# Optimization experiments

Hardware: AMD Instinct MI355X
Metric: run time of the kernel (lower is better)

The kernel has to match this reference:

```python
import jax, jax.numpy as jnp
import numpy as np

B, S, H, L = 4, 1024, 1024, 4
NH, NKV, HD = 16, 8, 64
F, V, W = 3072, 32000, 12
THETA = 1000000.0
EPS = 1e-6
NEG = -1e9


def _rms(x, w):
    return (x * jax.lax.rsqrt(jnp.mean(jnp.square(x), axis=-1, keepdims=True) + EPS)) * w


def _rotate_half(x):
    x1, x2 = jnp.split(x, 2, axis=-1)
    return jnp.concatenate([-x2, x1], axis=-1)


def setup_inputs() -> dict:
    key = jax.random.key(0)
    ks = jax.random.split(key, 16)
    s = 0.02
    return {
        'input_ids': jax.random.randint(ks[0], (B, S), 0, V),
        'attention_mask': jnp.ones((B, S), dtype=jnp.int32),
        'embed': jax.random.normal(ks[1], (V, H), jnp.float32) * s,
        'wq': jax.random.normal(ks[2], (L, H, NH * HD), jnp.float32) * s,
        'wk': jax.random.normal(ks[3], (L, H, NKV * HD), jnp.float32) * s,
        'wv': jax.random.normal(ks[4], (L, H, NKV * HD), jnp.float32) * s,
        'wo': jax.random.normal(ks[5], (L, NH * HD, H), jnp.float32) * s,
        'q_norm_w': jnp.ones((L, HD), jnp.float32),
        'k_norm_w': jnp.ones((L, HD), jnp.float32),
        'ln1': jnp.ones((L, H), jnp.float32),
        'ln2': jnp.ones((L, H), jnp.float32),
        'w_gate': jax.random.normal(ks[6], (L, H, F), jnp.float32) * s,
        'w_up': jax.random.normal(ks[7], (L, H, F), jnp.float32) * s,
        'w_down': jax.random.normal(ks[8], (L, F, H), jnp.float32) * s,
        'final_norm': jnp.ones((H,), jnp.float32),
    }


def _forward(embed, wq, wk, wv, wo, q_norm_w, k_norm_w, ln1, ln2,
             w_gate, w_up, w_down, final_norm, input_ids, attention_mask):
    h = embed[input_ids]                                   # [B,S,H]
    # rotary embeddings (Qwen3 style, theta=1e6)
    pos = jnp.arange(S, dtype=jnp.float32)
    inv_freq = 1.0 / (THETA ** (jnp.arange(0, HD, 2, dtype=jnp.float32) / HD))
    freqs = pos[:, None] * inv_freq[None, :]               # [S, HD/2]
    emb = jnp.concatenate([freqs, freqs], axis=-1)         # [S, HD]
    cos = jnp.cos(emb)[None, :, None, :]
    sin = jnp.sin(emb)[None, :, None, :]
    # masks: full = expanded (non-causal) padding mask; sliding = +/-W band
    pad = (1.0 - attention_mask.astype(jnp.float32))[:, None, None, :] * NEG
    idx = jnp.arange(S)
    band = jnp.abs(idx[:, None] - idx[None, :]) <= W       # [S,S]
    full_mask = jnp.broadcast_to(pad, (B, 1, S, S))
    slide_mask = jnp.where(band[None, None], full_mask, NEG)
    scale = 1.0 / np.sqrt(HD).astype(np.float32)
    for l in range(L):
        mask = full_mask if l % 2 == 0 else slide_mask     # attention_type dispatch
        x = _rms(h, ln1[l])
        q = _rms((x @ wq[l]).reshape(B, S, NH, HD), q_norm_w[l])
        k = _rms((x @ wk[l]).reshape(B, S, NKV, HD), k_norm_w[l])
        v = (x @ wv[l]).reshape(B, S, NKV, HD)
        q = q * cos + _rotate_half(q) * sin
        k = k * cos + _rotate_half(k) * sin
        rep = NH // NKV                                    # GQA expand
        k = jnp.repeat(k, rep, axis=2)
        v = jnp.repeat(v, rep, axis=2)
        scores = jnp.einsum('bqhd,bkhd->bhqk', q, k) * scale + mask
        p = jax.nn.softmax(scores, axis=-1)
        attn = jnp.einsum('bhqk,bkhd->bqhd', p, v).reshape(B, S, NH * HD)
        h = h + attn @ wo[l]
        x = _rms(h, ln2[l])
        h = h + (jax.nn.silu(x @ w_gate[l]) * (x @ w_up[l])) @ w_down[l]
    return _rms(h, final_norm)


def reference(input_ids, attention_mask, embed, wq, wk, wv, wo, q_norm_w, k_norm_w,
              ln1, ln2, w_gate, w_up, w_down, final_norm):
    return _forward(embed, wq, wk, wv, wo, q_norm_w, k_norm_w, ln1, ln2,
                    w_gate, w_up, w_down, final_norm, input_ids, attention_mask)
```

## Files before the change

### kernel.cpp

```cpp
#include <hip/hip_runtime.h>
#include <math.h>

#define BB 4
#define SS 1024
#define HH 1024
#define LL 4
#define NHH 16
#define NKV 8
#define HD 64
#define FF 3072
#define WW 12
#define NEG_INF (-1e9f)

typedef __attribute__((ext_vector_type(8))) short bf16x8;
typedef __attribute__((ext_vector_type(4))) float f32x4;
typedef __attribute__((ext_vector_type(16))) float f32x16;
typedef __attribute__((ext_vector_type(8))) unsigned short u16x8;

__device__ __forceinline__ unsigned short f2bf(float f) {
    union { float f; unsigned int u; } v; v.f = f;
    unsigned int r = (v.u + 0x7fffu + ((v.u >> 16) & 1u)) >> 16;
    return (unsigned short)r;
}
__device__ __forceinline__ float bf2f(unsigned short u) {
    union { unsigned int u; float f; } v; v.u = ((unsigned int)u) << 16;
    return v.f;
}
__device__ __forceinline__ unsigned int pkbf(float lo, float hi) {
    return (unsigned int)f2bf(lo) | ((unsigned int)f2bf(hi) << 16);
}
__device__ __forceinline__ void gll16(const void* g, void* l) {
    __builtin_amdgcn_global_load_lds((const __attribute__((address_space(1))) void*)g,
                                     (__attribute__((address_space(3))) void*)l, 16, 0, 0);
}

__global__ __launch_bounds__(256) void k_embed(const int* __restrict__ ids,
                                               const float* __restrict__ embed,
                                               float* __restrict__ h) {
    int row = blockIdx.x, tid = threadIdx.x;
    int id = ids[row];
    ((float4*)(h + (size_t)row * HH))[tid] = ((const float4*)(embed + (size_t)id * HH))[tid];
}

__global__ __launch_bounds__(256) void k_rms(const float* __restrict__ in,
                                             const float* __restrict__ w,
                                             float* __restrict__ out) {
    __shared__ float red[4];
    int row = blockIdx.x, tid = threadIdx.x;
    float4 v = ((const float4*)(in + (size_t)row * HH))[tid];
    float ss = v.x * v.x + v.y * v.y + v.z * v.z + v.w * v.w;
#pragma unroll
    for (int off = 1; off < 64; off <<= 1) ss += __shfl_xor(ss, off);
    if ((tid & 63) == 0) red[tid >> 6] = ss;
    __syncthreads();
    float tot = red[0] + red[1] + red[2] + red[3];
    float scale = rsqrtf(tot * (1.0f / HH) + 1e-6f);
    float4 wv = ((const float4*)w)[tid];
    float4 o;
    o.x = v.x * scale * wv.x; o.y = v.y * scale * wv.y;
    o.z = v.z * scale * wv.z; o.w = v.w * scale * wv.w;
    ((float4*)(out + (size_t)row * HH))[tid] = o;
}

__global__ __launch_bounds__(256) void k_rms_bf16(const float* __restrict__ in,
                                                  const float* __restrict__ w,
                                                  unsigned short* __restrict__ out) {
    __shared__ float red[4];
    int row = blockIdx.x, tid = threadIdx.x;
    float4 v = ((const float4*)(in + (size_t)row * HH))[tid];
    float ss = v.x * v.x + v.y * v.y + v.z * v.z + v.w * v.w;
#pragma unroll
    for (int off = 1; off < 64; off <<= 1) ss += __shfl_xor(ss, off);
    if ((tid & 63) == 0) red[tid >> 6] = ss;
    __syncthreads();
    float tot = red[0] + red[1] + red[2] + red[3];
    float scale = rsqrtf(tot * (1.0f / HH) + 1e-6f);
    float4 wv = ((const float4*)w)[tid];
    ushort4 o;
    o.x = f2bf(v.x * scale * wv.x); o.y = f2bf(v.y * scale * wv.y);
    o.z = f2bf(v.z * scale * wv.z); o.w = f2bf(v.w * scale * wv.w);
    *(ushort4*)&out[(size_t)row * HH + tid * 4] = o;
}

__global__ __launch_bounds__(256) void k_cast_t(const float* __restrict__ W,
                                                unsigned short* __restrict__ Wt,
                                                int N, int K) {
    __shared__ float t[64][65];
    int n0 = blockIdx.x * 64, k0 = blockIdx.y * 64;
    int tid = threadIdx.x;
    int r = tid >> 4;
    int c4 = (tid & 15) * 4;
#pragma unroll
    for (int e = 0; e < 4; ++e) {
        int kk = r + e * 16;
        float4 vv = *(const float4*)&W[(size_t)(k0 + kk) * N + n0 + c4];
        t[c4 + 0][kk] = vv.x;
        t[c4 + 1][kk] = vv.y;
        t[c4 + 2][kk] = vv.z;
        t[c4 + 3][kk] = vv.w;
    }
    __syncthreads();
#pragma unroll
    for (int e = 0; e < 4; ++e) {
        int nn = r + e * 16;
        ushort4 o;
        o.x = f2bf(t[nn][c4 + 0]);
        o.y = f2bf(t[nn][c4 + 1]);
        o.z = f2bf(t[nn][c4 + 2]);
        o.w = f2bf(t[nn][c4 + 3]);
        *(ushort4*)&Wt[(size_t)(n0 + nn) * K + k0 + c4] = o;
    }
}

template <int EPI>
__device__ __forceinline__ void mgemm_core(const unsigned short* __restrict__ A,
                                           const unsigned short* __restrict__ Bt,
                                           void* __restrict__ Cv,
                                           int N, int K, int bm, int bn) {
    __shared__ unsigned short As[128 * 32];
    __shared__ unsigned short Bs[128 * 32];
    int tid = threadIdx.x;
    int w = tid >> 6, l = tid & 63;
    int wr = (w >> 1) * 64, wc = (w & 1) * 64;

    f32x4 acc[4][4] = {};

    for (int k0 = 0; k0 < K; k0 += 32) {
        __syncthreads();
#pragma unroll
        for (int i = 0; i < 2; ++i) {
            int cb = i * 256 + w * 64;
            int c = cb + l;
            const unsigned short* ga = A + (size_t)(bm + (c >> 2)) * K + k0 + (c & 3) * 8;
            const unsigned short* gb = Bt + (size_t)(bn + (c >> 2)) * K + k0 + (c & 3) * 8;
            gll16(ga, As + cb * 8);
            gll16(gb, Bs + cb * 8);
        }
        __syncthreads();

        bf16x8 af[4], bfr[4];
#pragma unroll
        for (int i = 0; i < 4; ++i) {
            int m = wr + i * 16 + (l & 15);
            af[i] = *(const bf16x8*)&As[m * 32 + (l >> 4) * 8];
            int n = wc + i * 16 + (l & 15);
            bfr[i] = *(const bf16x8*)&Bs[n * 32 + (l >> 4) * 8];
        }
#pragma unroll
        for (int i = 0; i < 4; ++i)
#pragma unroll
            for (int j = 0; j < 4; ++j)
                acc[i][j] = __builtin_amdgcn_mfma_f32_16x16x32_bf16(af[i], bfr[j], acc[i][j], 0, 0, 0);
    }

#pragma unroll
    for (int i = 0; i < 4; ++i) {
        int rbase = bm + wr + i * 16 + (l >> 4) * 4;
#pragma unroll
        for (int j = 0; j < 4; ++j) {
            int col = bn + wc + j * 16 + (l & 15);
#pragma unroll
            for (int r = 0; r < 4; ++r) {
                size_t off = (size_t)(rbase + r) * N + col;
                if (EPI == 0) ((float*)Cv)[off] = acc[i][j][r];
                else if (EPI == 1) ((float*)Cv)[off] += acc[i][j][r];
                else ((unsigned short*)Cv)[off] = f2bf(acc[i][j][r]);
            }
        }
    }
}

template <int EPI>
__global__ __launch_bounds__(256) void k_mgemm(const unsigned short* __restrict__ A,
                                               const unsigned short* __restrict__ Bt,
                                               void* __restrict__ C,
                                               int N, int K) {
    mgemm_core<EPI>(A, Bt, C, N, K, blockIdx.y * 128, blockIdx.x * 128);
}

__global__ __launch_bounds__(256) void k_mgemm_qkv(const unsigned short* __restrict__ A,
                                                   const unsigned short* __restrict__ wqt,
                                                   const unsigned short* __restrict__ wkt,
                                                   const unsigned short* __restrict__ wvt,
                                                   float* __restrict__ q,
                                                   float* __restrict__ k,
                                                   unsigned short* __restrict__ v) {
    int nt = blockIdx.x;
    if (nt < 8)       mgemm_core<0>(A, wqt, q, 1024, 1024, blockIdx.y * 128, nt * 128);
    else if (nt < 12) mgemm_core<0>(A, wkt, k, 512, 1024, blockIdx.y * 128, (nt - 8) * 128);
    else              mgemm_core<2>(A, wvt, v, 512, 1024, blockIdx.y * 128, (nt - 12) * 128);
}

__global__ __launch_bounds__(256) void k_mgemm_gu(const unsigned short* __restrict__ A,
                                                  const unsigned short* __restrict__ wgt,
                                                  const unsigned short* __restrict__ wut,
                                                  unsigned short* __restrict__ g,
                                                  unsigned short* __restrict__ u) {
    int nt = blockIdx.x;
    const unsigned short* Bt = (nt < 24) ? wgt : wut;
    unsigned short* C = (nt < 24) ? g : u;
    int bn = (nt < 24 ? nt : nt - 24) * 128;
    mgemm_core<2>(A, Bt, C, 3072, 1024, blockIdx.y * 128, bn);
}

__global__ __launch_bounds__(256) void k_qknorm_rope(const float* __restrict__ qk,
                                                     unsigned short* __restrict__ out,
                                                     const float* __restrict__ nw,
                                                     int nheads) {
    int tid = threadIdx.x;
    int w = tid >> 6, lane = tid & 63;
    int gid = blockIdx.x * 4 + w;
    int row = gid / nheads;
    int pos = row & (SS - 1);
    size_t base = (size_t)gid * HD;
    float xv = qk[base + lane];
    float ss = xv * xv;
#pragma unroll
    for (int off = 1; off < 64; off <<= 1) ss += __shfl_xor(ss, off);
    float scale = rsqrtf(ss * (1.0f / HD) + 1e-6f);
    float xn = xv * scale * nw[lane];
    int j = lane & 31;
    float inv_freq = powf(1.0e6f, -(float)j * (1.0f / 32.0f));
    float f = (float)pos * inv_freq;
    float c = cosf(f), s = sinf(f);
    float partner = __shfl_xor(xn, 32);
    float rot = (lane < 32) ? -partner : partner;
    out[base + lane] = f2bf(xn * c + rot * s);
}

__global__ __launch_bounds__(256) void k_mattn(const unsigned short* __restrict__ q,
                                               const unsigned short* __restrict__ k,
                                               const unsigned short* __restrict__ v,
                                               const int* __restrict__ amask,
                                               unsigned short* __restrict__ out,
                                               int sliding) {
    __shared__ __align__(16) char smem[18432];
    unsigned short* Klds = (unsigned short*)smem;
    unsigned int*   VtU  = (unsigned int*)(smem + 8192);
    float* mlds          = (float*)(smem + 17152);
    unsigned short* Olds = (unsigned short*)smem;

    const int b = blockIdx.z, head = blockIdx.y, q0 = blockIdx.x * 128;
    const int kvh = head >> 1;
    const int tid = threadIdx.x, w = tid >> 6, lane = tid & 63;
    const int h = lane >> 5, ln31 = lane & 31;
    const int qg = q0 + w * 32 + ln31;
    const float sscale = 0.125f;

    bf16x8 qf[4];
    const unsigned short* qrow = q + (size_t)(b * SS + qg) * 1024 + head * 64;
#pragma unroll
    for (int c = 0; c < 4; ++c) qf[c] = *(const bf16x8*)(qrow + c * 16 + h * 8);

    f32x16 O0 = {}, O1 = {};
    float m = -3.4e38f, l_sum = 0.0f;

    int t_lo = 0, t_hi = (SS >> 6) - 1;
    if (sliding) {
        int lo = q0 - WW; if (lo < 0) lo = 0;
        int hi = q0 + 127 + WW; if (hi > SS - 1) hi = SS - 1;
        t_lo = lo >> 6; t_hi = hi >> 6;
    }

    const int vd = tid & 63, vw = tid >> 6;

    for (int t = t_lo; t <= t_hi; ++t) {
        int kv0 = t << 6;
        __syncthreads();
        if (tid < 64) mlds[tid] = amask[b * SS + kv0 + tid] ? 0.0f : NEG_INF;
#pragma unroll
        for (int i = 0; i < 2; ++i) {
            int slot = i * 256 + w * 64 + lane;
            int row = slot >> 3, u = slot & 7;
            int ug = u ^ (row & 7);
            const unsigned short* src = k + (size_t)(b * SS + kv0 + row) * 512 + kvh * 64 + ug * 8;
            gll16(src, Klds + (size_t)slot * 8);
        }
        {
            const unsigned short* vsrc = v + (size_t)(b * SS + kv0 + vw * 16) * 512 + kvh * 64 + vd;
            unsigned short tmp[16];
#pragma unroll
            for (int kk = 0; kk < 16; ++kk) tmp[kk] = vsrc[(size_t)kk * 512];
#pragma unroll
            for (int j = 0; j < 8; ++j)
                VtU[vd * 35 + vw * 8 + j] =
                    (unsigned int)tmp[2 * j] | ((unsigned int)tmp[2 * j + 1] << 16);
        }
        __syncthreads();

        f32x16 a0 = {}, a1 = {};
#pragma unroll
        for (int c = 0; c < 4; ++c) {
            int u = (2 * c + h) ^ (ln31 & 7);
            bf16x8 k0 = *(const bf16x8*)&Klds[ln31 * 64 + u * 8];
            bf16x8 k1 = *(const bf16x8*)&Klds[(32 + ln31) * 64 + u * 8];
            a0 = __builtin_amdgcn_mfma_f32_32x32x16_bf16(k0, qf[c], a0, 0, 0, 0);
            a1 = __builtin_amdgcn_mfma_f32_32x32x16_bf16(k1, qf[c], a1, 0, 0, 0);
        }

        float tmax = -3.4e38f;
#pragma unroll
        for (int r = 0; r < 16; ++r) {
            int kl = (r & 3) + 8 * (r >> 2) + 4 * h;
            float mv0 = mlds[kl], mv1 = mlds[32 + kl];
            if (sliding) {
                int d0 = qg - (kv0 + kl); if (d0 < 0) d0 = -d0;
                int d1 = qg - (kv0 + 32 + kl); if (d1 < 0) d1 = -d1;
                if (d0 > WW) mv0 = NEG_INF;
                if (d1 > WW) mv1 = NEG_INF;
            }
            a0[r] = a0[r] * sscale + mv0;
            a1[r] = a1[r] * sscale + mv1;
            tmax = fmaxf(tmax, fmaxf(a0[r], a1[r]));
        }
        tmax = fmaxf(tmax, __shfl_xor(tmax, 32));
        float nm = fmaxf(m, tmax);
        float corr = __expf(m - nm);
        float tsum = 0.0f;
#pragma unroll
        for (int r = 0; r < 16; ++r) {
            a0[r] = __expf(a0[r] - nm);
            a1[r] = __expf(a1[r] - nm);
            tsum += a0[r] + a1[r];
        }
        tsum += __shfl_xor(tsum, 32);
        l_sum = l_sum * corr + tsum;
#pragma unroll
        for (int r = 0; r < 16; ++r) { O0[r] *= corr; O1[r] *= corr; }
        m = nm;

#pragma unroll
        for (int s = 0; s < 2; ++s) {
#pragma unroll
            for (int c2 = 0; c2 < 2; ++c2) {
                float p0v = s ? a1[8 * c2 + 0] : a0[8 * c2 + 0];
                float p1v = s ? a1[8 * c2 + 1] : a0[8 * c2 + 1];
                float p2v = s ? a1[8 * c2 + 2] : a0[8 * c2 + 2];
                float p3v = s ? a1[8 * c2 + 3] : a0[8 * c2 + 3];
                float p4v = s ? a1[8 * c2 + 4] : a0[8 * c2 + 4];
                float p5v = s ? a1[8 * c2 + 5] : a0[8 * c2 + 5];
                float p6v = s ? a1[8 * c2 + 6] : a0[8 * c2 + 6];
                float p7v = s ? a1[8 * c2 + 7] : a0[8 * c2 + 7];
                unsigned int A0 = pkbf(p0v, p1v);
                unsigned int A1 = pkbf(p2v, p3v);
                unsigned int A2 = pkbf(p4v, p5v);
                unsigned int A3 = pkbf(p6v, p7v);
                unsigned int pA0 = (unsigned int)__shfl_xor((int)A0, 32);
                unsigned int pA1 = (unsigned int)__shfl_xor((int)A1, 32);
                unsigned int pA2 = (unsigned int)__shfl_xor((int)A2, 32);
                unsigned int pA3 = (unsigned int)__shfl_xor((int)A3, 32);
                union { unsigned int u[4]; bf16x8 v; } pf;
                pf.u[0] = h ? pA2 : A0;
                pf.u[1] = h ? pA3 : A1;
                pf.u[2] = h ? A2 : pA0;
                pf.u[3] = h ? A3 : pA1;
#pragma unroll
                for (int dt = 0; dt < 2; ++dt) {
                    int base = (dt * 32 + ln31) * 35 + s * 16 + c2 * 8 + h * 4;
                    union { unsigned int u[4]; bf16x8 v; } vf;
                    vf.u[0] = VtU[base + 0];
                    vf.u[1] = VtU[base + 1];
                    vf.u[2] = VtU[base + 2];
                    vf.u[3] = VtU[base + 3];
                    if (dt == 0) O0 = __builtin_amdgcn_mfma_f32_32x32x16_bf16(vf.v, pf.v, O0, 0, 0, 0);
                    else         O1 = __builtin_amdgcn_mfma_f32_32x32x16_bf16(vf.v, pf.v, O1, 0, 0, 0);
                }
            }
        }
    }

    __syncthreads();
    float rl = 1.0f / l_sum;
    unsigned short* myO = Olds + w * 2240;
#pragma unroll
    for (int dt = 0; dt < 2; ++dt)
#pragma unroll
        for (int r = 0; r < 16; ++r) {
            int d = dt * 32 + (r & 3) + 8 * (r >> 2) + 4 * h;
            float val = (dt ? O1[r] : O0[r]) * rl;
            myO[ln31 * 70 + d] = f2bf(val);
        }
    int qr = lane >> 1, half = lane & 1;
    const unsigned int* osrc = (const unsigned int*)Olds + (size_t)w * 1120 + qr * 35 + half * 16;
    unsigned int vals[16];
#pragma unroll
    for (int j = 0; j < 16; ++j) vals[j] = osrc[j];
    unsigned short* dst = out + (size_t)(b * SS + q0 + w * 32 + qr) * 1024 + head * 64 + half * 32;
#pragma unroll
    for (int j = 0; j < 4; ++j)
        ((uint4*)dst)[j] = make_uint4(vals[4 * j], vals[4 * j + 1], vals[4 * j + 2], vals[4 * j + 3]);
}

__global__ __launch_bounds__(256) void k_silu_bf16(unsigned short* __restrict__ g,
                                                   const unsigned short* __restrict__ u) {
    int i = blockIdx.x * 256 + threadIdx.x;
    u16x8 gv = ((const u16x8*)g)[i];
    u16x8 uv = ((const u16x8*)u)[i];
    u16x8 o;
#pragma unroll
    for (int j = 0; j < 8; ++j) {
        float gf = bf2f(gv[j]), uf = bf2f(uv[j]);
        o[j] = f2bf(gf / (1.0f + __expf(-gf)) * uf);
    }
    ((u16x8*)g)[i] = o;
}

extern "C" void kernel_launch(void* const* d_in, const int* in_sizes, int n_in,
                              void* d_out, int out_size, void* d_ws, size_t ws_size,
                              hipStream_t stream) {
    const int* input_ids = (const int*)d_in[0];
    const int* amask     = (const int*)d_in[1];
    const float* embed   = (const float*)d_in[2];
    const float* wq      = (const float*)d_in[3];
    const float* wk      = (const float*)d_in[4];
    const float* wv      = (const float*)d_in[5];
    const float* wo      = (const float*)d_in[6];
    const float* qnw     = (const float*)d_in[7];
    const float* knw     = (const float*)d_in[8];
    const float* ln1     = (const float*)d_in[9];
    const float* ln2     = (const float*)d_in[10];
    const float* wg      = (const float*)d_in[11];
    const float* wu      = (const float*)d_in[12];
    const float* wd      = (const float*)d_in[13];
    const float* fnorm   = (const float*)d_in[14];
    float* out = (float*)d_out;

    const int ROWS = BB * SS;
    float* h  = (float*)d_ws;
    float* qb = h + (size_t)ROWS * HH;
    float* kb = qb + (size_t)ROWS * HH;
    unsigned short* xb  = (unsigned short*)(kb + (size_t)ROWS * (NKV * HD));
    unsigned short* qbf = xb + (size_t)ROWS * HH;
    unsigned short* kbf = qbf + (size_t)ROWS * HH;
    unsigned short* vbf = kbf + (size_t)ROWS * (NKV * HD);
    unsigned short* gbf = vbf + (size_t)ROWS * (NKV * HD);
    unsigned short* ubf = gbf + (size_t)ROWS * FF;
    unsigned short* wbf = ubf + (size_t)ROWS * FF;

    const size_t OQ = 0, OK_ = 1048576, OV = 1572864, OO = 2097152,
                 OG = 3145728, OU = 6291456, OD = 9437184;

    k_embed<<<ROWS, 256, 0, stream>>>(input_ids, embed, h);

    for (int l = 0; l < LL; ++l) {
        const float* wq_l = wq + (size_t)l * HH * (NHH * HD);
        const float* wk_l = wk + (size_t)l * HH * (NKV * HD);
        const float* wv_l = wv + (size_t)l * HH * (NKV * HD);
        const float* wo_l = wo + (size_t)l * (NHH * HD) * HH;
        const float* wg_l = wg + (size_t)l * HH * FF;
        const float* wu_l = wu + (size_t)l * HH * FF;
        const float* wd_l = wd + (size_t)l * FF * HH;

        k_cast_t<<<dim3(16, 16), 256, 0, stream>>>(wq_l, wbf + OQ, 1024, 1024);
        k_cast_t<<<dim3(8, 16),  256, 0, stream>>>(wk_l, wbf + OK_, 512, 1024);
        k_cast_t<<<dim3(8, 16),  256, 0, stream>>>(wv_l, wbf + OV, 512, 1024);
        k_cast_t<<<dim3(16, 16), 256, 0, stream>>>(wo_l, wbf + OO, 1024, 1024);
        k_cast_t<<<dim3(48, 16), 256, 0, stream>>>(wg_l, wbf + OG, 3072, 1024);
        k_cast_t<<<dim3(48, 16), 256, 0, stream>>>(wu_l, wbf + OU, 3072, 1024);
        k_cast_t<<<dim3(16, 48), 256, 0, stream>>>(wd_l, wbf + OD, 1024, 3072);

        k_rms_bf16<<<ROWS, 256, 0, stream>>>(h, ln1 + l * HH, xb);

        k_mgemm_qkv<<<dim3(16, 32), 256, 0, stream>>>(xb, wbf + OQ, wbf + OK_, wbf + OV,
                                                      qb, kb, vbf);

        k_qknorm_rope<<<ROWS * NHH / 4, 256, 0, stream>>>(qb, qbf, qnw + l * HD, NHH);
        k_qknorm_rope<<<ROWS * NKV / 4, 256, 0, stream>>>(kb, kbf, knw + l * HD, NKV);

        k_mattn<<<dim3(SS / 128, NHH, BB), 256, 0, stream>>>(qbf, kbf, vbf, amask, xb, l & 1);

        k_mgemm<1><<<dim3(8, 32), 256, 0, stream>>>(xb, wbf + OO, h, 1024, 1024);

        k_rms_bf16<<<ROWS, 256, 0, stream>>>(h, ln2 + l * HH, xb);

        k_mgemm_gu<<<dim3(48, 32), 256, 0, stream>>>(xb, wbf + OG, wbf + OU, gbf, ubf);

        k_silu_bf16<<<ROWS * FF / 8 / 256, 256, 0, stream>>>(gbf, ubf);

        k_mgemm<1><<<dim3(8, 32), 256, 0, stream>>>(gbf, wbf + OD, h, 1024, 3072);
    }

    k_rms<<<ROWS, 256, 0, stream>>>(h, fnorm, out);
}
```

Baseline: 1.571 ms.

## Split-K the wo and down GEMMs, fuse residual add into RMSNorm, merge weight casts

The output-projection and down-projection GEMMs are split along K into 2 and 3 parts. Each part writes float partials into scratch buffers that are no longer live (qb, gbf, ubf, part of wbf), which raises the block count above the 256-tile grid. A new fused kernel adds the partials to the residual stream and applies the next RMSNorm, including the first norm of the next layer and the final norm. The seven per-layer weight cast/transpose launches are merged into one launch. The cost is extra partial-buffer traffic and tighter buffer aliasing, which is fragile if the layout ever changes.

```diff
diff --git a/kernel.cpp b/kernel.cpp
--- a/kernel.cpp
+++ b/kernel.cpp
@@ -12,6 +12,14 @@
 #define WW 12
 #define NEG_INF (-1e9f)
 
+#define OQ  0
+#define OK_ 1048576
+#define OV  1572864
+#define OO  2097152
+#define OG  3145728
+#define OU  6291456
+#define OD  9437184
+
 typedef __attribute__((ext_vector_type(8))) short bf16x8;
 typedef __attribute__((ext_vector_type(4))) float f32x4;
 typedef __attribute__((ext_vector_type(16))) float f32x16;
@@ -40,26 +48,6 @@
     int row = blockIdx.x, tid = threadIdx.x;
     int id = ids[row];
     ((float4*)(h + (size_t)row * HH))[tid] = ((const float4*)(embed + (size_t)id * HH))[tid];
-}
-
-__global__ __launch_bounds__(256) void k_rms(const float* __restrict__ in,
-                                             const float* __restrict__ w,
-                                             float* __restrict__ out) {
-    __shared__ float red[4];
-    int row = blockIdx.x, tid = threadIdx.x;
-    float4 v = ((const float4*)(in + (size_t)row * HH))[tid];
-    float ss = v.x * v.x + v.y * v.y + v.z * v.z + v.w * v.w;
-#pragma unroll
-    for (int off = 1; off < 64; off <<= 1) ss += __shfl_xor(ss, off);
-    if ((tid & 63) == 0) red[tid >> 6] = ss;
-    __syncthreads();
-    float tot = red[0] + red[1] + red[2] + red[3];
-    float scale = rsqrtf(tot * (1.0f / HH) + 1e-6f);
-    float4 wv = ((const float4*)w)[tid];
-    float4 o;
-    o.x = v.x * scale * wv.x; o.y = v.y * scale * wv.y;
-    o.z = v.z * scale * wv.z; o.w = v.w * scale * wv.w;
-    ((float4*)(out + (size_t)row * HH))[tid] = o;
 }
 
 __global__ __launch_bounds__(256) void k_rms_bf16(const float* __restrict__ in,
@@ -82,11 +70,68 @@
     *(ushort4*)&out[(size_t)row * HH + tid * 4] = o;
 }
 
-__global__ __launch_bounds__(256) void k_cast_t(const float* __restrict__ W,
-                                                unsigned short* __restrict__ Wt,
-                                                int N, int K) {
+template <int NP, int BF16OUT>
+__global__ __launch_bounds__(256) void k_rms_add(float* __restrict__ h,
+                                                 const float* __restrict__ p0,
+                                                 const float* __restrict__ p1,
+                                                 const float* __restrict__ p2,
+                                                 const float* __restrict__ w,
+                                                 void* __restrict__ outx) {
+    __shared__ float red[4];
+    int row = blockIdx.x, tid = threadIdx.x;
+    size_t base = (size_t)row * HH;
+    float4 v = ((const float4*)(h + base))[tid];
+    float4 a = ((const float4*)(p0 + base))[tid];
+    v.x += a.x; v.y += a.y; v.z += a.z; v.w += a.w;
+    if (NP > 1) {
+        float4 b = ((const float4*)(p1 + base))[tid];
+        v.x += b.x; v.y += b.y; v.z += b.z; v.w += b.w;
+    }
+    if (NP > 2) {
+        float4 c = ((const float4*)(p2 + base))[tid];
+        v.x += c.x; v.y += c.y; v.z += c.z; v.w += c.w;
+    }
+    ((float4*)(h + base))[tid] = v;
+    float ss = v.x * v.x + v.y * v.y + v.z * v.z + v.w * v.w;
+#pragma unroll
+    for (int off = 1; off < 64; off <<= 1) ss += __shfl_xor(ss, off);
+    if ((tid & 63) == 0) red[tid >> 6] = ss;
+    __syncthreads();
+    float tot = red[0] + red[1] + red[2] + red[3];
+    float scale = rsqrtf(tot * (1.0f / HH) + 1e-6f);
+    float4 wv = ((const float4*)w)[tid];
+    float rx = v.x * scale * wv.x, ry = v.y * scale * wv.y;
+    float rz = v.z * scale * wv.z, rw = v.w * scale * wv.w;
+    if (BF16OUT) {
+        ushort4 o;
+        o.x = f2bf(rx); o.y = f2bf(ry); o.z = f2bf(rz); o.w = f2bf(rw);
+        *(ushort4*)&((unsigned short*)outx)[base + tid * 4] = o;
+    } else {
+        float4 o; o.x = rx; o.y = ry; o.z = rz; o.w = rw;
+        ((float4*)((float*)outx + base))[tid] = o;
+    }
+}
+
+__global__ __launch_bounds__(256) void k_cast_all(const float* __restrict__ wq,
+                                                  const float* __restrict__ wk,
+                                                  const float* __restrict__ wv,
+                                                  const float* __restrict__ wo,
+                                                  const float* __restrict__ wg,
+                                                  const float* __restrict__ wu,
+                                                  const float* __restrict__ wd,
+                                                  unsigned short* __restrict__ wbf) {
     __shared__ float t[64][65];
-    int n0 = blockIdx.x * 64, k0 = blockIdx.y * 64;
+    int tI = blockIdx.x;
+    const float* W; unsigned short* Wt; int N, K, local;
+    if (tI < 256)       { W = wq; Wt = wbf + OQ;  N = 1024; K = 1024; local = tI; }
+    else if (tI < 384)  { W = wk; Wt = wbf + OK_; N = 512;  K = 1024; local = tI - 256; }
+    else if (tI < 512)  { W = wv; Wt = wbf + OV;  N = 512;  K = 1024; local = tI - 384; }
+    else if (tI < 768)  { W = wo; Wt = wbf + OO;  N = 1024; K = 1024; local = tI - 512; }
+    else if (tI < 1536) { W = wg; Wt = wbf + OG;  N = 3072; K = 1024; local = tI - 768; }
+    else if (tI < 2304) { W = wu; Wt = wbf + OU;  N = 3072; K = 1024; local = tI - 1536; }
+    else                { W = wd; Wt = wbf + OD;  N = 1024; K = 3072; local = tI - 2304; }
+    int tn = N >> 6;
+    int n0 = (local % tn) * 64, k0 = (local / tn) * 64;
     int tid = threadIdx.x;
     int r = tid >> 4;
     int c4 = (tid & 15) * 4;
@@ -116,7 +161,8 @@
 __device__ __forceinline__ void mgemm_core(const unsigned short* __restrict__ A,
                                            const unsigned short* __restrict__ Bt,
                                            void* __restrict__ Cv,
-                                           int N, int K, int bm, int bn) {
+                                           int N, int K, int lda, int ldb,
+                                           int bm, int bn) {
     __shared__ unsigned short As[128 * 32];
     __shared__ unsigned short Bs[128 * 32];
     int tid = threadIdx.x;
@@ -131,8 +177,8 @@
         for (int i = 0; i < 2; ++i) {
             int cb = i * 256 + w * 64;
             int c = cb + l;
-            const unsigned short* ga = A + (size_t)(bm + (c >> 2)) * K + k0 + (c & 3) * 8;
-            const unsigned short* gb = Bt + (size_t)(bn + (c >> 2)) * K + k0 + (c & 3) * 8;
+            const unsigned short* ga = A + (size_t)(bm + (c >> 2)) * lda + k0 + (c & 3) * 8;
+            const unsigned short* gb = Bt + (size_t)(bn + (c >> 2)) * ldb + k0 + (c & 3) * 8;
             gll16(ga, As + cb * 8);
             gll16(gb, Bs + cb * 8);
         }
@@ -170,12 +216,18 @@
     }
 }
 
-template <int EPI>
-__global__ __launch_bounds__(256) void k_mgemm(const unsigned short* __restrict__ A,
-                                               const unsigned short* __restrict__ Bt,
-                                               void* __restrict__ C,
-                                               int N, int K) {
-    mgemm_core<EPI>(A, Bt, C, N, K, blockIdx.y * 128, blockIdx.x * 128);
+template <int PARTS>
+__global__ __launch_bounds__(256) void k_mgemm_splitk(const unsigned short* __restrict__ A,
+                                                      const unsigned short* __restrict__ Bt,
+                                                      float* __restrict__ p0,
+                                                      float* __restrict__ p1,
+                                                      float* __restrict__ p2,
+                                                      int N, int Ktot) {
+    int part = blockIdx.z;
+    int Kp = Ktot / PARTS;
+    float* C = (part == 0) ? p0 : (part == 1 ? p1 : p2);
+    mgemm_core<0>(A + part * Kp, Bt + part * Kp, C, N, Kp, Ktot, Ktot,
+                  blockIdx.y * 128, blockIdx.x * 128);
 }
 
 __global__ __launch_bounds__(256) void k_mgemm_qkv(const unsigned short* __restrict__ A,
@@ -186,9 +238,9 @@
                                                    float* __restrict__ k,
                                                    unsigned short* __restrict__ v) {
     int nt = blockIdx.x;
-    if (nt < 8)       mgemm_core<0>(A, wqt, q, 1024, 1024, blockIdx.y * 128, nt * 128);
-    else if (nt < 12) mgemm_core<0>(A, wkt, k, 512, 1024, blockIdx.y * 128, (nt - 8) * 128);
-    else              mgemm_core<2>(A, wvt, v, 512, 1024, blockIdx.y * 128, (nt - 12) * 128);
+    if (nt < 8)       mgemm_core<0>(A, wqt, q, 1024, 1024, 1024, 1024, blockIdx.y * 128, nt * 128);
+    else if (nt < 12) mgemm_core<0>(A, wkt, k, 512, 1024, 1024, 1024, blockIdx.y * 128, (nt - 8) * 128);
+    else              mgemm_core<2>(A, wvt, v, 512, 1024, 1024, 1024, blockIdx.y * 128, (nt - 12) * 128);
 }
 
 __global__ __launch_bounds__(256) void k_mgemm_gu(const unsigned short* __restrict__ A,
@@ -200,7 +252,7 @@
     const unsigned short* Bt = (nt < 24) ? wgt : wut;
     unsigned short* C = (nt < 24) ? g : u;
     int bn = (nt < 24 ? nt : nt - 24) * 128;
-    mgemm_core<2>(A, Bt, C, 3072, 1024, blockIdx.y * 128, bn);
+    mgemm_core<2>(A, Bt, C, 3072, 1024, 1024, 1024, blockIdx.y * 128, bn);
 }
 
 __global__ __launch_bounds__(256) void k_qknorm_rope(const float* __restrict__ qk,
@@ -437,10 +489,8 @@
     unsigned short* ubf = gbf + (size_t)ROWS * FF;
     unsigned short* wbf = ubf + (size_t)ROWS * FF;
 
-    const size_t OQ = 0, OK_ = 1048576, OV = 1572864, OO = 2097152,
-                 OG = 3145728, OU = 6291456, OD = 9437184;
-
     k_embed<<<ROWS, 256, 0, stream>>>(input_ids, embed, h);
+    k_rms_bf16<<<ROWS, 256, 0, stream>>>(h, ln1, xb);
 
     for (int l = 0; l < LL; ++l) {
         const float* wq_l = wq + (size_t)l * HH * (NHH * HD);
@@ -451,15 +501,7 @@
         const float* wu_l = wu + (size_t)l * HH * FF;
         const float* wd_l = wd + (size_t)l * FF * HH;
 
-        k_cast_t<<<dim3(16, 16), 256, 0, stream>>>(wq_l, wbf + OQ, 1024, 1024);
-        k_cast_t<<<dim3(8, 16),  256, 0, stream>>>(wk_l, wbf + OK_, 512, 1024);
-        k_cast_t<<<dim3(8, 16),  256, 0, stream>>>(wv_l, wbf + OV, 512, 1024);
-        k_cast_t<<<dim3(16, 16), 256, 0, stream>>>(wo_l, wbf + OO, 1024, 1024);
-        k_cast_t<<<dim3(48, 16), 256, 0, stream>>>(wg_l, wbf + OG, 3072, 1024);
-        k_cast_t<<<dim3(48, 16), 256, 0, stream>>>(wu_l, wbf + OU, 3072, 1024);
-        k_cast_t<<<dim3(16, 48), 256, 0, stream>>>(wd_l, wbf + OD, 1024, 3072);
-
-        k_rms_bf16<<<ROWS, 256, 0, stream>>>(h, ln1 + l * HH, xb);
+        k_cast_all<<<3072, 256, 0, stream>>>(wq_l, wk_l, wv_l, wo_l, wg_l, wu_l, wd_l, wbf);
 
         k_mgemm_qkv<<<dim3(16, 32), 256, 0, stream>>>(xb, wbf + OQ, wbf + OK_, wbf + OV,
                                                       qb, kb, vbf);
@@ -469,16 +511,23 @@
 
         k_mattn<<<dim3(SS / 128, NHH, BB), 256, 0, stream>>>(qbf, kbf, vbf, amask, xb, l & 1);
 
-        k_mgemm<1><<<dim3(8, 32), 256, 0, stream>>>(xb, wbf + OO, h, 1024, 1024);
-
-        k_rms_bf16<<<ROWS, 256, 0, stream>>>(h, ln2 + l * HH, xb);
+        k_mgemm_splitk<2><<<dim3(8, 32, 2), 256, 0, stream>>>(xb, wbf + OO, qb, (float*)gbf,
+                                                              nullptr, 1024, 1024);
+        k_rms_add<2, 1><<<ROWS, 256, 0, stream>>>(h, qb, (float*)gbf, nullptr,
+                                                  ln2 + l * HH, xb);
 
         k_mgemm_gu<<<dim3(48, 32), 256, 0, stream>>>(xb, wbf + OG, wbf + OU, gbf, ubf);
 
         k_silu_bf16<<<ROWS * FF / 8 / 256, 256, 0, stream>>>(gbf, ubf);
 
-        k_mgemm<1><<<dim3(8, 32), 256, 0, stream>>>(gbf, wbf + OD, h, 1024, 3072);
-    }
-
-    k_rms<<<ROWS, 256, 0, stream>>>(h, fnorm, out);
-}
+        k_mgemm_splitk<3><<<dim3(8, 32, 3), 256, 0, stream>>>(gbf, wbf + OD, qb, (float*)ubf,
+                                                              (float*)wbf, 1024, 3072);
+        if (l < LL - 1) {
+            k_rms_add<3, 1><<<ROWS, 256, 0, stream>>>(h, qb, (float*)ubf, (float*)wbf,
+                                                      ln1 + (l + 1) * HH, xb);
+        } else {
+            k_rms_add<3, 0><<<ROWS, 256, 0, stream>>>(h, qb, (float*)ubf, (float*)wbf,
+                                                      fnorm, out);
+        }
+    }
+}
```

Measured after the change: 1.412 ms. 1.11x faster.
